# Kernel tuning notes

Measured on AMD Instinct MI355X. Metric: run time of the kernel, lower is better.

Reference implementation:

```python
import jax, jax.numpy as jnp
import numpy as np

HIDDEN = 4096
N_HEADS = 32
N_KV_HEADS = 8
HEAD_DIM = HIDDEN // N_HEADS  # 128
ROPE_THETA = 10000.0


def _rotate_half(x):
    x1, x2 = jnp.split(x, 2, axis=-1)
    return jnp.concatenate([-x2, x1], axis=-1)


def setup_inputs() -> dict:
    key = jax.random.key(0)
    ks = jax.random.split(key, 6)
    B, S = 1, 2048
    hidden_states = jax.random.normal(ks[0], (B, S, HIDDEN), jnp.float32) * 0.02
    # additive causal mask [B,1,S,S] as the HF attention_mask the module expects
    i = jnp.arange(S)
    attention_mask = jnp.where(i[:, None] >= i[None, :], 0.0, -1e9).astype(jnp.float32)[None, None]
    position_ids = jnp.arange(S, dtype=jnp.int32)[None, :]
    w_scale = 0.02
    Wq = jax.random.normal(ks[1], (N_HEADS * HEAD_DIM, HIDDEN), jnp.float32) * w_scale
    Wk = jax.random.normal(ks[2], (N_KV_HEADS * HEAD_DIM, HIDDEN), jnp.float32) * w_scale
    Wv = jax.random.normal(ks[3], (N_KV_HEADS * HEAD_DIM, HIDDEN), jnp.float32) * w_scale
    Wo = jax.random.normal(ks[4], (HIDDEN, N_HEADS * HEAD_DIM), jnp.float32) * w_scale
    return {
        "hidden_states": hidden_states,
        "attention_mask": attention_mask,
        "position_ids": position_ids,
        "Wq": Wq, "Wk": Wk, "Wv": Wv, "Wo": Wo,
    }


def reference(hidden_states, attention_mask, position_ids, Wq, Wk, Wv, Wo):
    B, S, _ = hidden_states.shape
    # projections (bias=False)
    q = (hidden_states @ Wq.T).reshape(B, S, N_HEADS, HEAD_DIM).transpose(0, 2, 1, 3)
    k = (hidden_states @ Wk.T).reshape(B, S, N_KV_HEADS, HEAD_DIM).transpose(0, 2, 1, 3)
    v = (hidden_states @ Wv.T).reshape(B, S, N_KV_HEADS, HEAD_DIM).transpose(0, 2, 1, 3)
    # rotary embedding
    inv_freq = 1.0 / (ROPE_THETA ** (jnp.arange(0, HEAD_DIM, 2, dtype=jnp.float32) / HEAD_DIM))
    t = jnp.arange(S, dtype=jnp.float32)
    freqs = t[:, None] * inv_freq[None, :]            # [S, HEAD_DIM/2]
    emb = jnp.concatenate([freqs, freqs], axis=-1)    # [S, HEAD_DIM]
    cos = jnp.cos(emb)[position_ids][:, None]         # [B,1,S,HEAD_DIM]
    sin = jnp.sin(emb)[position_ids][:, None]
    q = q * cos + _rotate_half(q) * sin
    k = k * cos + _rotate_half(k) * sin
    # repeat_kv for GQA
    groups = N_HEADS // N_KV_HEADS
    k = jnp.repeat(k, groups, axis=1)
    v = jnp.repeat(v, groups, axis=1)
    # QK^T / sqrt(d) + mask, fp32 softmax
    scores = jnp.einsum("bhqd,bhkd->bhqk", q, k) / np.sqrt(HEAD_DIM).astype(np.float32)
    scores = scores + attention_mask
    attn = jax.nn.softmax(scores.astype(jnp.float32), axis=-1).astype(q.dtype)
    out = jnp.einsum("bhqk,bhkd->bhqd", attn, v)
    out = out.transpose(0, 2, 1, 3).reshape(B, S, N_HEADS * HEAD_DIM)
    return out @ Wo.T
```

## Files before the change

### kernel.cpp

```cpp
#include <hip/hip_runtime.h>
#include <stdint.h>

#define HIDDEN 4096
#define SEQ    2048
#define NH     32
#define NKV    8
#define HD     128
#define QKVN   (HIDDEN + 2 * NKV * HD)

typedef __attribute__((ext_vector_type(8))) short short8;
typedef __attribute__((ext_vector_type(4))) float float4v;
typedef __attribute__((ext_vector_type(4))) unsigned short ushort4v;
typedef unsigned short bf16_t;

__device__ __forceinline__ bf16_t f2bf(float f) {
  unsigned u = __builtin_bit_cast(unsigned, f);
  u += 0x7fff + ((u >> 16) & 1);
  return (bf16_t)(u >> 16);
}
__device__ __forceinline__ float bf2f(bf16_t h) {
  unsigned u = ((unsigned)h) << 16;
  return __builtin_bit_cast(float, u);
}

__device__ __forceinline__ void gload_lds16(const void* g, void* l) {
  __builtin_amdgcn_global_load_lds(
      (const __attribute__((address_space(1))) unsigned int*)g,
      (__attribute__((address_space(3))) unsigned int*)l, 16, 0, 0);
}

__global__ __launch_bounds__(256) void cvt_f32_bf16(const float* __restrict__ src,
                                                    bf16_t* __restrict__ dst) {
  long i = ((long)blockIdx.x * 256 + threadIdx.x) * 4;
  float4v f = *(const float4v*)(src + i);
  ushort4v o;
  o.x = f2bf(f.x); o.y = f2bf(f.y); o.z = f2bf(f.z); o.w = f2bf(f.w);
  *(ushort4v*)(dst + i) = o;
}

__global__ __launch_bounds__(256) void rope_kernel(bf16_t* __restrict__ x,
                                                   const int* __restrict__ pos,
                                                   int n_heads, int row_stride) {
  long tid = (long)blockIdx.x * 256 + threadIdx.x;
  int j = (int)(tid & 63);
  long sh = tid >> 6;
  int s = (int)(sh / n_heads);
  int hh = (int)(sh % n_heads);
  bf16_t* row = x + (long)s * row_stride + hh * 128;
  float f = (float)pos[s] * exp2f((float)j * (-13.28771237954945f / 64.f));
  float sn, cs;
  __sincosf(f, &sn, &cs);
  float a = bf2f(row[j]), b = bf2f(row[j + 64]);
  row[j]      = f2bf(a * cs - b * sn);
  row[j + 64] = f2bf(b * cs + a * sn);
}

__global__ __launch_bounds__(256) void transpose_v(const bf16_t* __restrict__ v,
                                                   bf16_t* __restrict__ vt,
                                                   int src_stride, int col_off) {
  __shared__ __align__(16) bf16_t tile[64][72];
  int s0 = blockIdx.x * 64, c0 = blockIdx.y * 64;
  int t = threadIdx.x;
#pragma unroll
  for (int j = 0; j < 8; ++j) {
    int u = j * 256 + t;
    int sl = u >> 5, dl = (u & 31) * 2;
    unsigned val = *(const unsigned*)(v + (long)(s0 + sl) * src_stride + col_off + c0 + dl);
    tile[sl][dl] = (bf16_t)(val & 0xffff);
    tile[sl][dl + 1] = (bf16_t)(val >> 16);
  }
  __syncthreads();
  int kvh = c0 >> 7, dbase = c0 & 127;
#pragma unroll
  for (int j = 0; j < 8; ++j) {
    int u = j * 256 + t;
    int dl = u >> 5, sl = (u & 31) * 2;
    unsigned val = (unsigned)tile[sl][dl] | ((unsigned)tile[sl + 1][dl] << 16);
    *(unsigned*)(vt + (long)kvh * HD * SEQ + (long)(dbase + dl) * SEQ + s0 + sl) = val;
  }
}

template <int OUTF32>
__global__ __launch_bounds__(256) void gemm_bt(const bf16_t* __restrict__ A,
                                               const bf16_t* __restrict__ B,
                                               void* __restrict__ Cp,
                                               int M, int N, int K) {
  __shared__ __align__(16) bf16_t As[128 * 32];
  __shared__ __align__(16) bf16_t Bs[128 * 32];
  const int tid = threadIdx.x;
  const int w = tid >> 6, lane = tid & 63;
  const int bm = blockIdx.y, bn = blockIdx.x;
  const int wr = (w >> 1) * 64, wc = (w & 1) * 64;
  float4v acc[4][4] = {};
  const bf16_t* gA = A + (long)bm * 128 * K;
  const bf16_t* gB = B + (long)bn * 128 * K;
  const int c0 = w * 2, c1 = w * 2 + 1;
  const int rsub = lane >> 2, csub = (lane & 3) * 8;
  const int lr = lane & 15, lk = (lane >> 4) * 8;

  for (int k0 = 0; k0 < K; k0 += 32) {
    gload_lds16(gA + (long)(c0 * 16 + rsub) * K + k0 + csub, &As[c0 * 512]);
    gload_lds16(gA + (long)(c1 * 16 + rsub) * K + k0 + csub, &As[c1 * 512]);
    gload_lds16(gB + (long)(c0 * 16 + rsub) * K + k0 + csub, &Bs[c0 * 512]);
    gload_lds16(gB + (long)(c1 * 16 + rsub) * K + k0 + csub, &Bs[c1 * 512]);
    asm volatile("s_waitcnt vmcnt(0)" ::: "memory");
    __syncthreads();
    short8 af[4], bfr[4];
#pragma unroll
    for (int i = 0; i < 4; ++i)
      af[i] = *(const short8*)&As[(wr + i * 16 + lr) * 32 + lk];
#pragma unroll
    for (int i = 0; i < 4; ++i)
      bfr[i] = *(const short8*)&Bs[(wc + i * 16 + lr) * 32 + lk];
#pragma unroll
    for (int mi = 0; mi < 4; ++mi)
#pragma unroll
      for (int ni = 0; ni < 4; ++ni)
        acc[mi][ni] = __builtin_amdgcn_mfma_f32_16x16x32_bf16(af[mi], bfr[ni], acc[mi][ni], 0, 0, 0);
    __syncthreads();
  }
  const int lq = (lane >> 4) * 4;
#pragma unroll
  for (int mi = 0; mi < 4; ++mi)
#pragma unroll
    for (int ni = 0; ni < 4; ++ni) {
      int row = bm * 128 + wr + mi * 16 + lq;
      int col = bn * 128 + wc + ni * 16 + lr;
#pragma unroll
      for (int r = 0; r < 4; ++r) {
        float vv = acc[mi][ni][r];
        if (OUTF32)
          ((float*)Cp)[(long)(row + r) * N + col] = vv;
        else
          ((bf16_t*)Cp)[(long)(row + r) * N + col] = f2bf(vv);
      }
    }
}

__global__ __launch_bounds__(256, 2) void attn_kernel(const bf16_t* __restrict__ QKV,
                                                      const bf16_t* __restrict__ Vt,
                                                      bf16_t* __restrict__ O) {
  __shared__ __align__(16) bf16_t Ks[64 * 128];
  __shared__ __align__(16) bf16_t Vs[128 * 64];
  __shared__ __align__(16) bf16_t Ps[4 * 16 * 88];
  const int tid = threadIdx.x, w = tid >> 6, lane = tid & 63;
  const int h = blockIdx.y;
  const int x = blockIdx.x;
  const int qt = (x & 1) ? (SEQ / 128 - 1 - (x >> 1)) : (x >> 1);
  const int kvh = h >> 2;
  const int q0 = qt * 128 + w * 32;
  const int ktmax = 2 * qt + 1;
  const int lr = lane & 15, lkb = lane >> 4;
  const float scale = 0.08838834764831845f;
  const bf16_t* Kbase = QKV + HIDDEN + kvh * HD;

  short8 qf[2][4];
#pragma unroll
  for (int qs = 0; qs < 2; ++qs)
#pragma unroll
    for (int kb = 0; kb < 4; ++kb)
      qf[qs][kb] = *(const short8*)(QKV + (long)(q0 + qs * 16 + lr) * QKVN + h * HD + kb * 32 + lkb * 8);

  float4v acc_o[2][8] = {};
  float mrow[2][4], lrow[2][4];
#pragma unroll
  for (int qs = 0; qs < 2; ++qs)
#pragma unroll
    for (int r = 0; r < 4; ++r) { mrow[qs][r] = -1e30f; lrow[qs][r] = 0.f; }

  for (int kt = 0; kt <= ktmax; ++kt) {
    __syncthreads();
#pragma unroll
    for (int j = 0; j < 4; ++j) {
      int c = tid + j * 256;
      int row = c >> 4, d0 = (c & 15) * 8;
      float4v kv = *(const float4v*)(Kbase + (long)(kt * 64 + row) * QKVN + d0);
      int byte = (row * 256 + d0 * 2) ^ ((row & 7) << 4);
      *(float4v*)((char*)Ks + byte) = kv;
    }
#pragma unroll
    for (int j = 0; j < 4; ++j) {
      int c = tid + j * 256;
      int d = c >> 3, key0 = (c & 7) * 8;
      float4v vv = *(const float4v*)(Vt + (long)kvh * HD * SEQ + (long)d * SEQ + kt * 64 + key0);
      int byte = (d * 128 + key0 * 2) ^ ((d & 7) << 4);
      *(float4v*)((char*)Vs + byte) = vv;
    }
    __syncthreads();

#pragma unroll
    for (int qs = 0; qs < 2; ++qs) {
      const int q0s = q0 + qs * 16;
      const int st_kt = q0s >> 6;
      if (kt > st_kt) continue;

      float4v accs[4] = {};
      __builtin_amdgcn_s_setprio(1);
#pragma unroll
      for (int c = 0; c < 4; ++c) {
#pragma unroll
        for (int kb = 0; kb < 4; ++kb) {
          int row = c * 16 + lr;
          int byte = (row * 256 + (kb * 32 + lkb * 8) * 2) ^ ((row & 7) << 4);
          short8 kf = *(const short8*)((char*)Ks + byte);
          accs[c] = __builtin_amdgcn_mfma_f32_16x16x32_bf16(qf[qs][kb], kf, accs[c], 0, 0, 0);
        }
      }
      __builtin_amdgcn_s_setprio(0);

      const bool diag = (kt == st_kt);
      float p[4][4];
      float pm[4];
#pragma unroll
      for (int r = 0; r < 4; ++r) pm[r] = -1e30f;
#pragma unroll
      for (int c = 0; c < 4; ++c)
#pragma unroll
        for (int r = 0; r < 4; ++r) {
          float s = accs[c][r] * scale;
          if (diag) {
            int key = kt * 64 + c * 16 + lr;
            int qrow = q0s + lkb * 4 + r;
            if (key > qrow) s = -1e30f;
          }
          p[c][r] = s;
          pm[r] = fmaxf(pm[r], s);
        }
#pragma unroll
      for (int r = 0; r < 4; ++r) {
        float v = pm[r];
        v = fmaxf(v, __shfl_xor(v, 1));
        v = fmaxf(v, __shfl_xor(v, 2));
        v = fmaxf(v, __shfl_xor(v, 4));
        v = fmaxf(v, __shfl_xor(v, 8));
        float mnew = fmaxf(mrow[qs][r], v);
        float alpha = __expf(mrow[qs][r] - mnew);
        mrow[qs][r] = mnew;
        lrow[qs][r] *= alpha;
#pragma unroll
        for (int dj = 0; dj < 8; ++dj) acc_o[qs][dj][r] *= alpha;
      }
      float psum[4] = {0.f, 0.f, 0.f, 0.f};
#pragma unroll
      for (int c = 0; c < 4; ++c)
#pragma unroll
        for (int r = 0; r < 4; ++r) {
          float e = __expf(p[c][r] - mrow[qs][r]);
          p[c][r] = e;
          psum[r] += e;
        }
#pragma unroll
      for (int r = 0; r < 4; ++r) {
        float v = psum[r];
        v += __shfl_xor(v, 1);
        v += __shfl_xor(v, 2);
        v += __shfl_xor(v, 4);
        v += __shfl_xor(v, 8);
        lrow[qs][r] += v;
      }
      bf16_t* ps = &Ps[w * 16 * 88];
#pragma unroll
      for (int c = 0; c < 4; ++c)
#pragma unroll
        for (int r = 0; r < 4; ++r)
          ps[(lkb * 4 + r) * 88 + c * 16 + lr] = f2bf(p[c][r]);
      short8 pf[2];
#pragma unroll
      for (int kb2 = 0; kb2 < 2; ++kb2)
        pf[kb2] = *(const short8*)&ps[lr * 88 + kb2 * 32 + lkb * 8];
      __builtin_amdgcn_s_setprio(1);
#pragma unroll
      for (int dj = 0; dj < 8; ++dj) {
#pragma unroll
        for (int kb2 = 0; kb2 < 2; ++kb2) {
          int d = dj * 16 + lr;
          int byte = (d * 128 + (kb2 * 32 + lkb * 8) * 2) ^ ((d & 7) << 4);
          short8 vf = *(const short8*)((char*)Vs + byte);
          acc_o[qs][dj] = __builtin_amdgcn_mfma_f32_16x16x32_bf16(pf[kb2], vf, acc_o[qs][dj], 0, 0, 0);
        }
      }
      __builtin_amdgcn_s_setprio(0);
    }
  }
#pragma unroll
  for (int qs = 0; qs < 2; ++qs)
#pragma unroll
    for (int dj = 0; dj < 8; ++dj)
#pragma unroll
      for (int r = 0; r < 4; ++r) {
        float v = acc_o[qs][dj][r] / lrow[qs][r];
        O[(long)(q0 + qs * 16 + lkb * 4 + r) * HIDDEN + h * HD + dj * 16 + lr] = f2bf(v);
      }
}

extern "C" void kernel_launch(void* const* d_in, const int* in_sizes, int n_in,
                              void* d_out, int out_size, void* d_ws, size_t ws_size,
                              hipStream_t stream) {
  const float* hs  = (const float*)d_in[0];
  const int* pos   = (const int*)d_in[2];
  const float* Wq  = (const float*)d_in[3];
  const float* Wk  = (const float*)d_in[4];
  const float* Wv  = (const float*)d_in[5];
  const float* Wo  = (const float*)d_in[6];
  float* out       = (float*)d_out;

  char* ws = (char*)d_ws;
  const long MB = 1024 * 1024;
  bf16_t* hsb   = (bf16_t*)(ws + 0);
  bf16_t* wqkvb = (bf16_t*)(ws + 16 * MB);
  bf16_t* wob   = (bf16_t*)(ws + 64 * MB);
  bf16_t* qkvb  = (bf16_t*)(ws + 96 * MB);
  bf16_t* vtb   = (bf16_t*)(ws + 120 * MB);
  bf16_t* aob   = (bf16_t*)(ws + 124 * MB);

  cvt_f32_bf16<<<(SEQ * HIDDEN) / 1024, 256, 0, stream>>>(hs, hsb);
  cvt_f32_bf16<<<(HIDDEN * HIDDEN) / 1024, 256, 0, stream>>>(Wq, wqkvb);
  cvt_f32_bf16<<<(NKV * HD * HIDDEN) / 1024, 256, 0, stream>>>(Wk, wqkvb + (long)HIDDEN * HIDDEN);
  cvt_f32_bf16<<<(NKV * HD * HIDDEN) / 1024, 256, 0, stream>>>(Wv, wqkvb + (long)(HIDDEN + NKV * HD) * HIDDEN);
  cvt_f32_bf16<<<(HIDDEN * HIDDEN) / 1024, 256, 0, stream>>>(Wo, wob);

  gemm_bt<0><<<dim3(QKVN / 128, SEQ / 128), 256, 0, stream>>>(hsb, wqkvb, qkvb, SEQ, QKVN, HIDDEN);

  rope_kernel<<<(SEQ * NH * 64) / 256, 256, 0, stream>>>(qkvb, pos, NH, QKVN);
  rope_kernel<<<(SEQ * NKV * 64) / 256, 256, 0, stream>>>(qkvb + HIDDEN, pos, NKV, QKVN);

  transpose_v<<<dim3(SEQ / 64, (NKV * HD) / 64), 256, 0, stream>>>(qkvb, vtb, QKVN, HIDDEN + NKV * HD);

  attn_kernel<<<dim3(SEQ / 128, NH), 256, 0, stream>>>(qkvb, vtb, aob);

  gemm_bt<1><<<dim3(HIDDEN / 128, SEQ / 128), 256, 0, stream>>>(aob, wob, out, SEQ, HIDDEN, HIDDEN);
}
```

Before: 622.3 us.

## Restructure attention with atomic task queue, transposed MFMA and lazy rescale

The attention kernel switches to a persistent-style loop that takes (q-tile, head) tasks from a global atomic counter, heaviest causal tiles first, to balance load. It swaps MFMA operand order so each lane holds a full query row, which removes the cross-lane max/sum shuffles for 16 lanes. It also processes both 16-row query subtiles together, uses exp2 with the log2e folded into the scale, skips the rescale unless the running max grows past a threshold, and packs bf16 with v_cvt_pk_bf16. The costs are an extra memset, an atomic per task, and the numerical risk of deferred rescaling.

```diff
diff --git a/kernel.cpp b/kernel.cpp
--- a/kernel.cpp
+++ b/kernel.cpp
@@ -7,10 +7,12 @@
 #define NKV    8
 #define HD     128
 #define QKVN   (HIDDEN + 2 * NKV * HD)
+#define NTASK  512
 
 typedef __attribute__((ext_vector_type(8))) short short8;
 typedef __attribute__((ext_vector_type(4))) float float4v;
 typedef __attribute__((ext_vector_type(4))) unsigned short ushort4v;
+typedef __attribute__((ext_vector_type(2))) unsigned int uint2v;
 typedef unsigned short bf16_t;
 
 __device__ __forceinline__ bf16_t f2bf(float f) {
@@ -21,6 +23,11 @@
 __device__ __forceinline__ float bf2f(bf16_t h) {
   unsigned u = ((unsigned)h) << 16;
   return __builtin_bit_cast(float, u);
+}
+__device__ __forceinline__ unsigned cvt_pk_bf16(float lo, float hi) {
+  unsigned r;
+  asm("v_cvt_pk_bf16_f32 %0, %1, %2" : "=v"(r) : "v"(lo), "v"(hi));
+  return r;
 }
 
 __device__ __forceinline__ void gload_lds16(const void* g, void* l) {
@@ -139,158 +146,161 @@
 
 __global__ __launch_bounds__(256, 2) void attn_kernel(const bf16_t* __restrict__ QKV,
                                                       const bf16_t* __restrict__ Vt,
-                                                      bf16_t* __restrict__ O) {
+                                                      bf16_t* __restrict__ O,
+                                                      int* __restrict__ ctr) {
   __shared__ __align__(16) bf16_t Ks[64 * 128];
   __shared__ __align__(16) bf16_t Vs[128 * 64];
-  __shared__ __align__(16) bf16_t Ps[4 * 16 * 88];
+  __shared__ __align__(16) bf16_t Ps[8][16 * 72];
+  __shared__ int s_task;
   const int tid = threadIdx.x, w = tid >> 6, lane = tid & 63;
-  const int h = blockIdx.y;
-  const int x = blockIdx.x;
-  const int qt = (x & 1) ? (SEQ / 128 - 1 - (x >> 1)) : (x >> 1);
-  const int kvh = h >> 2;
-  const int q0 = qt * 128 + w * 32;
-  const int ktmax = 2 * qt + 1;
-  const int lr = lane & 15, lkb = lane >> 4;
-  const float scale = 0.08838834764831845f;
-  const bf16_t* Kbase = QKV + HIDDEN + kvh * HD;
-
-  short8 qf[2][4];
-#pragma unroll
-  for (int qs = 0; qs < 2; ++qs)
-#pragma unroll
-    for (int kb = 0; kb < 4; ++kb)
-      qf[qs][kb] = *(const short8*)(QKV + (long)(q0 + qs * 16 + lr) * QKVN + h * HD + kb * 32 + lkb * 8);
-
-  float4v acc_o[2][8] = {};
-  float mrow[2][4], lrow[2][4];
-#pragma unroll
-  for (int qs = 0; qs < 2; ++qs)
-#pragma unroll
-    for (int r = 0; r < 4; ++r) { mrow[qs][r] = -1e30f; lrow[qs][r] = 0.f; }
-
-  for (int kt = 0; kt <= ktmax; ++kt) {
+  const int lr = lane & 15, g = lane >> 4;
+  const float kscale = 0.1275310246f;
+
+  for (;;) {
     __syncthreads();
-#pragma unroll
-    for (int j = 0; j < 4; ++j) {
-      int c = tid + j * 256;
-      int row = c >> 4, d0 = (c & 15) * 8;
-      float4v kv = *(const float4v*)(Kbase + (long)(kt * 64 + row) * QKVN + d0);
-      int byte = (row * 256 + d0 * 2) ^ ((row & 7) << 4);
-      *(float4v*)((char*)Ks + byte) = kv;
-    }
-#pragma unroll
-    for (int j = 0; j < 4; ++j) {
-      int c = tid + j * 256;
-      int d = c >> 3, key0 = (c & 7) * 8;
-      float4v vv = *(const float4v*)(Vt + (long)kvh * HD * SEQ + (long)d * SEQ + kt * 64 + key0);
-      int byte = (d * 128 + key0 * 2) ^ ((d & 7) << 4);
-      *(float4v*)((char*)Vs + byte) = vv;
-    }
+    if (tid == 0) s_task = atomicAdd(ctr, 1);
     __syncthreads();
-
-#pragma unroll
-    for (int qs = 0; qs < 2; ++qs) {
-      const int q0s = q0 + qs * 16;
-      const int st_kt = q0s >> 6;
+    const int t = s_task;
+    if (t >= NTASK) return;
+    const int qt = 15 - (t >> 5);
+    const int h = t & 31, kvh = h >> 2;
+    const int q0 = qt * 128 + w * 32;
+    const int st_kt = q0 >> 6;
+    const int ktmax = 2 * qt + 1;
+    const bf16_t* Kb = QKV + HIDDEN + kvh * HD;
+    const bf16_t* Vb = Vt + (long)kvh * HD * SEQ;
+
+    short8 qf[2][4];
+#pragma unroll
+    for (int qs = 0; qs < 2; ++qs)
+#pragma unroll
+      for (int kb = 0; kb < 4; ++kb)
+        qf[qs][kb] = *(const short8*)(QKV + (long)(q0 + qs * 16 + lr) * QKVN + h * HD + kb * 32 + g * 8);
+
+    float4v acc_o[2][8] = {};
+    float mrow[2] = {-1e30f, -1e30f}, lrow[2] = {0.f, 0.f};
+
+    for (int kt = 0; kt <= ktmax; ++kt) {
+      __syncthreads();
+#pragma unroll
+      for (int j = 0; j < 4; ++j) {
+        int c = tid + j * 256;
+        int row = c >> 4, d0 = (c & 15) * 8;
+        float4v kv = *(const float4v*)(Kb + (long)(kt * 64 + row) * QKVN + d0);
+        int byte = (row * 256 + d0 * 2) ^ ((row & 7) << 4);
+        *(float4v*)((char*)Ks + byte) = kv;
+      }
+#pragma unroll
+      for (int j = 0; j < 4; ++j) {
+        int c = tid + j * 256;
+        int d = c >> 3, key0 = (c & 7) * 8;
+        float4v vv = *(const float4v*)(Vb + (long)d * SEQ + kt * 64 + key0);
+        int byte = (d * 128 + key0 * 2) ^ ((d & 7) << 4);
+        *(float4v*)((char*)Vs + byte) = vv;
+      }
+      __syncthreads();
+
       if (kt > st_kt) continue;
-
-      float4v accs[4] = {};
+      const bool diag = (kt == st_kt);
+
+      float4v accs[2][4] = {};
       __builtin_amdgcn_s_setprio(1);
 #pragma unroll
       for (int c = 0; c < 4; ++c) {
 #pragma unroll
         for (int kb = 0; kb < 4; ++kb) {
           int row = c * 16 + lr;
-          int byte = (row * 256 + (kb * 32 + lkb * 8) * 2) ^ ((row & 7) << 4);
+          int byte = (row * 256 + (kb * 32 + g * 8) * 2) ^ ((row & 7) << 4);
           short8 kf = *(const short8*)((char*)Ks + byte);
-          accs[c] = __builtin_amdgcn_mfma_f32_16x16x32_bf16(qf[qs][kb], kf, accs[c], 0, 0, 0);
+          accs[0][c] = __builtin_amdgcn_mfma_f32_16x16x32_bf16(kf, qf[0][kb], accs[0][c], 0, 0, 0);
+          accs[1][c] = __builtin_amdgcn_mfma_f32_16x16x32_bf16(kf, qf[1][kb], accs[1][c], 0, 0, 0);
         }
       }
       __builtin_amdgcn_s_setprio(0);
 
-      const bool diag = (kt == st_kt);
-      float p[4][4];
-      float pm[4];
-#pragma unroll
-      for (int r = 0; r < 4; ++r) pm[r] = -1e30f;
-#pragma unroll
-      for (int c = 0; c < 4; ++c)
-#pragma unroll
-        for (int r = 0; r < 4; ++r) {
-          float s = accs[c][r] * scale;
-          if (diag) {
-            int key = kt * 64 + c * 16 + lr;
-            int qrow = q0s + lkb * 4 + r;
-            if (key > qrow) s = -1e30f;
+      short8 pf[2][2];
+#pragma unroll
+      for (int qs = 0; qs < 2; ++qs) {
+        const int qrow = q0 + qs * 16 + lr;
+        float p[4][4];
+        float pm = -1e30f;
+#pragma unroll
+        for (int c = 0; c < 4; ++c)
+#pragma unroll
+          for (int r = 0; r < 4; ++r) {
+            float s = accs[qs][c][r] * kscale;
+            if (diag) {
+              int key = kt * 64 + c * 16 + g * 4 + r;
+              if (key > qrow) s = -1e30f;
+            }
+            p[c][r] = s;
+            pm = fmaxf(pm, s);
           }
-          p[c][r] = s;
-          pm[r] = fmaxf(pm[r], s);
-        }
-#pragma unroll
-      for (int r = 0; r < 4; ++r) {
-        float v = pm[r];
-        v = fmaxf(v, __shfl_xor(v, 1));
-        v = fmaxf(v, __shfl_xor(v, 2));
-        v = fmaxf(v, __shfl_xor(v, 4));
-        v = fmaxf(v, __shfl_xor(v, 8));
-        float mnew = fmaxf(mrow[qs][r], v);
-        float alpha = __expf(mrow[qs][r] - mnew);
-        mrow[qs][r] = mnew;
-        lrow[qs][r] *= alpha;
-#pragma unroll
-        for (int dj = 0; dj < 8; ++dj) acc_o[qs][dj][r] *= alpha;
-      }
-      float psum[4] = {0.f, 0.f, 0.f, 0.f};
-#pragma unroll
-      for (int c = 0; c < 4; ++c)
-#pragma unroll
-        for (int r = 0; r < 4; ++r) {
-          float e = __expf(p[c][r] - mrow[qs][r]);
-          p[c][r] = e;
-          psum[r] += e;
-        }
-#pragma unroll
-      for (int r = 0; r < 4; ++r) {
-        float v = psum[r];
-        v += __shfl_xor(v, 1);
-        v += __shfl_xor(v, 2);
-        v += __shfl_xor(v, 4);
-        v += __shfl_xor(v, 8);
-        lrow[qs][r] += v;
-      }
-      bf16_t* ps = &Ps[w * 16 * 88];
-#pragma unroll
-      for (int c = 0; c < 4; ++c)
-#pragma unroll
-        for (int r = 0; r < 4; ++r)
-          ps[(lkb * 4 + r) * 88 + c * 16 + lr] = f2bf(p[c][r]);
-      short8 pf[2];
-#pragma unroll
-      for (int kb2 = 0; kb2 < 2; ++kb2)
-        pf[kb2] = *(const short8*)&ps[lr * 88 + kb2 * 32 + lkb * 8];
+        pm = fmaxf(pm, __shfl_xor(pm, 16));
+        pm = fmaxf(pm, __shfl_xor(pm, 32));
+        if (__any(pm > mrow[qs] + 11.5f)) {
+          float mnew = fmaxf(mrow[qs], pm);
+          float alpha = exp2f(mrow[qs] - mnew);
+          mrow[qs] = mnew;
+          lrow[qs] *= alpha;
+#pragma unroll
+          for (int dj = 0; dj < 8; ++dj) acc_o[qs][dj] *= alpha;
+        }
+        float psum = 0.f;
+#pragma unroll
+        for (int c = 0; c < 4; ++c)
+#pragma unroll
+          for (int r = 0; r < 4; ++r) {
+            float e = exp2f(p[c][r] - mrow[qs]);
+            p[c][r] = e;
+            psum += e;
+          }
+        psum += __shfl_xor(psum, 16);
+        psum += __shfl_xor(psum, 32);
+        lrow[qs] += psum;
+        char* psB = (char*)Ps[w * 2 + qs];
+#pragma unroll
+        for (int c = 0; c < 4; ++c) {
+          uint2v pk;
+          pk.x = cvt_pk_bf16(p[c][0], p[c][1]);
+          pk.y = cvt_pk_bf16(p[c][2], p[c][3]);
+          int byte = (lr * 144 + c * 32 + g * 8) ^ ((lr & 1) << 4);
+          *(uint2v*)(psB + byte) = pk;
+        }
+#pragma unroll
+        for (int kb2 = 0; kb2 < 2; ++kb2) {
+          int byte = (lr * 144 + kb2 * 64 + g * 16) ^ ((lr & 1) << 4);
+          pf[qs][kb2] = *(const short8*)(psB + byte);
+        }
+      }
+
       __builtin_amdgcn_s_setprio(1);
 #pragma unroll
       for (int dj = 0; dj < 8; ++dj) {
 #pragma unroll
         for (int kb2 = 0; kb2 < 2; ++kb2) {
           int d = dj * 16 + lr;
-          int byte = (d * 128 + (kb2 * 32 + lkb * 8) * 2) ^ ((d & 7) << 4);
+          int byte = (d * 128 + (kb2 * 32 + g * 8) * 2) ^ ((d & 7) << 4);
           short8 vf = *(const short8*)((char*)Vs + byte);
-          acc_o[qs][dj] = __builtin_amdgcn_mfma_f32_16x16x32_bf16(pf[kb2], vf, acc_o[qs][dj], 0, 0, 0);
+          acc_o[0][dj] = __builtin_amdgcn_mfma_f32_16x16x32_bf16(vf, pf[0][kb2], acc_o[0][dj], 0, 0, 0);
+          acc_o[1][dj] = __builtin_amdgcn_mfma_f32_16x16x32_bf16(vf, pf[1][kb2], acc_o[1][dj], 0, 0, 0);
         }
       }
       __builtin_amdgcn_s_setprio(0);
     }
+
+#pragma unroll
+    for (int qs = 0; qs < 2; ++qs) {
+      float rl = 1.0f / lrow[qs];
+#pragma unroll
+      for (int dj = 0; dj < 8; ++dj) {
+        uint2v pk;
+        pk.x = cvt_pk_bf16(acc_o[qs][dj][0] * rl, acc_o[qs][dj][1] * rl);
+        pk.y = cvt_pk_bf16(acc_o[qs][dj][2] * rl, acc_o[qs][dj][3] * rl);
+        *(uint2v*)(&O[(long)(q0 + qs * 16 + lr) * HIDDEN + h * HD + dj * 16 + g * 4]) = pk;
+      }
+    }
   }
-#pragma unroll
-  for (int qs = 0; qs < 2; ++qs)
-#pragma unroll
-    for (int dj = 0; dj < 8; ++dj)
-#pragma unroll
-      for (int r = 0; r < 4; ++r) {
-        float v = acc_o[qs][dj][r] / lrow[qs][r];
-        O[(long)(q0 + qs * 16 + lkb * 4 + r) * HIDDEN + h * HD + dj * 16 + lr] = f2bf(v);
-      }
 }
 
 extern "C" void kernel_launch(void* const* d_in, const int* in_sizes, int n_in,
@@ -312,6 +322,9 @@
   bf16_t* qkvb  = (bf16_t*)(ws + 96 * MB);
   bf16_t* vtb   = (bf16_t*)(ws + 120 * MB);
   bf16_t* aob   = (bf16_t*)(ws + 124 * MB);
+  int*    ctr   = (int*)(ws + 140 * MB);
+
+  hipMemsetAsync(ctr, 0, 4, stream);
 
   cvt_f32_bf16<<<(SEQ * HIDDEN) / 1024, 256, 0, stream>>>(hs, hsb);
   cvt_f32_bf16<<<(HIDDEN * HIDDEN) / 1024, 256, 0, stream>>>(Wq, wqkvb);
@@ -326,7 +339,7 @@
 
   transpose_v<<<dim3(SEQ / 64, (NKV * HD) / 64), 256, 0, stream>>>(qkvb, vtb, QKVN, HIDDEN + NKV * HD);
 
-  attn_kernel<<<dim3(SEQ / 128, NH), 256, 0, stream>>>(qkvb, vtb, aob);
+  attn_kernel<<<NTASK, 256, 0, stream>>>(qkvb, vtb, aob, ctr);
 
   gemm_bt<1><<<dim3(HIDDEN / 128, SEQ / 128), 256, 0, stream>>>(aob, wob, out, SEQ, HIDDEN, HIDDEN);
 }
```

After: 575.8 us. -7.5%, faster.
